# Kernel tuning notes

Measured on AMD Instinct MI355X. Metric: run time of the kernel, lower is better.

The kernel has to match this reference:

```python
import jax, jax.numpy as jnp
import numpy as np

B, S, D_MODEL, H = 2, 2048, 1024, 16
HD = D_MODEL // H  # 64
EPS = 1e-6


def setup_inputs() -> dict:
    key = jax.random.key(0)
    ks = jax.random.split(key, 8)
    x = jax.random.normal(ks[0], (B, S, D_MODEL), dtype=jnp.float32)
    # Proper RoPE rotation angles: theta_i = pos / 10000^(2i/head_dim)
    inv_freq = 1.0 / (10000.0 ** (np.arange(0, HD, 2, dtype=np.float32) / HD))  # (HD/2,)
    angles = np.arange(S, dtype=np.float32)[:, None] * inv_freq[None, :]        # (S, HD/2)
    rope_cos = jnp.asarray(np.cos(angles))
    rope_sin = jnp.asarray(np.sin(angles))
    w_std = 1.0 / np.sqrt(D_MODEL)
    wq = jax.random.normal(ks[1], (D_MODEL, D_MODEL), dtype=jnp.float32) * w_std
    wk = jax.random.normal(ks[2], (D_MODEL, D_MODEL), dtype=jnp.float32) * w_std
    wv = jax.random.normal(ks[3], (D_MODEL, D_MODEL), dtype=jnp.float32) * w_std
    wo = jax.random.normal(ks[4], (D_MODEL, D_MODEL), dtype=jnp.float32) * w_std
    q_scale = 1.0 + 0.02 * jax.random.normal(ks[5], (HD,), dtype=jnp.float32)
    k_scale = 1.0 + 0.02 * jax.random.normal(ks[6], (HD,), dtype=jnp.float32)
    return {"x": x, "wq": wq, "wk": wk, "wv": wv, "wo": wo,
            "q_scale": q_scale, "k_scale": k_scale,
            "rope_cos": rope_cos, "rope_sin": rope_sin}


def _rmsnorm(t, scale):
    # RMSNorm over head_dim
    var = jnp.mean(jnp.square(t), axis=-1, keepdims=True)
    return t * jax.lax.rsqrt(var + EPS) * scale


def _apply_rope(t, cos, sin):
    # t: (B,S,H,HD); interpret consecutive pairs as complex (real, imag)
    b, s, h, d = t.shape
    tp = t.reshape(b, s, h, d // 2, 2)
    tr, ti = tp[..., 0], tp[..., 1]
    c = cos[None, :, None, :]  # (1,S,1,HD/2)
    sn = sin[None, :, None, :]
    or_ = tr * c - ti * sn
    oi = tr * sn + ti * c
    return jnp.stack([or_, oi], axis=-1).reshape(b, s, h, d)


def reference(x, wq, wk, wv, wo, q_scale, k_scale, rope_cos, rope_sin):
    b, s, _ = x.shape
    # Torch-style linear: y = x @ W^T, W is (out, in)
    q = jnp.einsum('bsd,od->bso', x, wq).reshape(b, s, H, HD)
    k = jnp.einsum('bsd,od->bso', x, wk).reshape(b, s, H, HD)
    v = jnp.einsum('bsd,od->bso', x, wv).reshape(b, s, H, HD)
    q = _apply_rope(_rmsnorm(q, q_scale), rope_cos, rope_sin)
    k = _apply_rope(_rmsnorm(k, k_scale), rope_cos, rope_sin)
    # scaled dot-product attention (no mask), fp32 softmax
    scale = 1.0 / np.sqrt(HD)
    scores = jnp.einsum('bqhd,bkhd->bhqk', q, k) * scale
    probs = jax.nn.softmax(scores.astype(jnp.float32), axis=-1)
    attn = jnp.einsum('bhqk,bkhd->bqhd', probs, v).reshape(b, s, D_MODEL)
    return jnp.einsum('bso,do->bsd', attn, wo.T).astype(x.dtype) if False else jnp.einsum('bsd,od->bso', attn, wo)
```

## Files before the change

kernel.cpp:

```cpp
#include <hip/hip_runtime.h>
#include <hip/hip_bf16.h>


#define B_ 2
#define S_ 2048
#define D_ 1024
#define H_ 16
#define HD_ 64
#define M_ (B_*S_)
#define SPLIT_ 2
#define KSPAN_ (S_/SPLIT_)

typedef __attribute__((ext_vector_type(8))) short short8;
typedef __attribute__((ext_vector_type(4))) short short4v;
typedef __attribute__((ext_vector_type(4))) float f32x4;
typedef __attribute__((ext_vector_type(4))) _Float16 half4;
typedef __attribute__((ext_vector_type(8))) _Float16 half8;

static __device__ __forceinline__ short f2bf(float f) {
    __hip_bfloat16 h = __float2bfloat16(f);
    return *reinterpret_cast<short*>(&h);
}
static __device__ __forceinline__ short f2h(float f) {
    _Float16 h = (_Float16)f;
    return *reinterpret_cast<short*>(&h);
}

typedef __attribute__((address_space(1))) const unsigned int gu32_t;
typedef __attribute__((address_space(3))) unsigned int lu32_t;
static __device__ __forceinline__ void gld16(const short* g, short* l) {
    __builtin_amdgcn_global_load_lds((gu32_t*)g, (lu32_t*)l, 16, 0, 0);
}

__global__ __launch_bounds__(256)
void convert_bf16(const float* __restrict__ x,
                  const float* __restrict__ wq, const float* __restrict__ wk,
                  const float* __restrict__ wv, const float* __restrict__ wo,
                  short* __restrict__ xb, short* __restrict__ wqkvb, short* __restrict__ wob)
{
    const size_t t4 = ((size_t)blockIdx.x * 256 + threadIdx.x) * 4;
    const float* src; short* dst; size_t off, doff;
    if (t4 < 4194304)      { src = x;  dst = xb;    off = t4;           doff = t4; }
    else if (t4 < 5242880) { src = wq; dst = wqkvb; off = t4 - 4194304; doff = t4 - 4194304; }
    else if (t4 < 6291456) { src = wk; dst = wqkvb; off = t4 - 5242880; doff = t4 - 4194304; }
    else if (t4 < 7340032) { src = wv; dst = wqkvb; off = t4 - 6291456; doff = t4 - 4194304; }
    else                   { src = wo; dst = wob;   off = t4 - 7340032; doff = t4 - 7340032; }
    float4 v = *(const float4*)(src + off);
    short4v s = { f2bf(v.x), f2bf(v.y), f2bf(v.z), f2bf(v.w) };
    *(short4v*)(dst + doff) = s;
}

__global__ __launch_bounds__(256)
void gemm_qkv(const short* __restrict__ A, const short* __restrict__ Bw,
              short* __restrict__ Qb, short* __restrict__ Kb, short* __restrict__ Vt,
              const float* __restrict__ q_scale, const float* __restrict__ k_scale,
              const float* __restrict__ rope_cos, const float* __restrict__ rope_sin)
{
    __shared__ __align__(16) short As[2][128*64];
    __shared__ __align__(16) short Bs[2][128*64];
    const int tid = threadIdx.x;
    const int w = tid >> 6, lane = tid & 63, quad = lane >> 4, l16 = lane & 15;
    const int wr = w >> 1, wc = w & 1;
    const int bm0 = blockIdx.x * 128, bn0 = blockIdx.y * 128;

    const int row_ = tid >> 3;
    const int kslot = tid & 7;
    const short* gA[4]; const short* gB[4];
    #pragma unroll
    for (int j = 0; j < 4; ++j) {
        const int row = j*32 + row_;
        const int kch = kslot ^ (row & 7);
        gA[j] = A  + (size_t)(bm0 + row) * 1024 + kch*8;
        gB[j] = Bw + (size_t)(bn0 + row) * 1024 + kch*8;
    }

    f32x4 acc[4][4];
    #pragma unroll
    for (int i = 0; i < 4; ++i)
        #pragma unroll
        for (int j = 0; j < 4; ++j) acc[i][j] = (f32x4){0.f,0.f,0.f,0.f};

    #pragma unroll
    for (int j = 0; j < 4; ++j) {
        gld16(gA[j], &As[0][j*2048 + w*512]);
        gld16(gB[j], &Bs[0][j*2048 + w*512]);
    }
    asm volatile("s_waitcnt vmcnt(0)" ::: "memory");
    __builtin_amdgcn_s_barrier();
    __builtin_amdgcn_sched_barrier(0);

    int cur = 0;
    for (int t = 0; t < 16; ++t) {
        if (t < 15) {
            const int k0 = (t + 1) * 64;
            #pragma unroll
            for (int j = 0; j < 4; ++j) {
                gld16(gA[j] + k0, &As[cur ^ 1][j*2048 + w*512]);
                gld16(gB[j] + k0, &Bs[cur ^ 1][j*2048 + w*512]);
            }
        }
        __builtin_amdgcn_sched_barrier(0);

        short8 af[2][4], bfr[2][4];
        #pragma unroll
        for (int ph = 0; ph < 2; ++ph)
            #pragma unroll
            for (int i = 0; i < 4; ++i) {
                const int ra = wr*64 + i*16 + l16;
                af[ph][i]  = *(const short8*)(&As[cur][ra*64 + (((ph*4 + quad) ^ (ra & 7)) << 3)]);
                const int rb = wc*64 + i*16 + l16;
                bfr[ph][i] = *(const short8*)(&Bs[cur][rb*64 + (((ph*4 + quad) ^ (rb & 7)) << 3)]);
            }
        #pragma unroll
        for (int ph = 0; ph < 2; ++ph)
            #pragma unroll
            for (int i = 0; i < 4; ++i)
                #pragma unroll
                for (int j = 0; j < 4; ++j)
                    acc[i][j] = __builtin_amdgcn_mfma_f32_16x16x32_bf16(af[ph][i], bfr[ph][j], acc[i][j], 0, 0, 0);

        asm volatile("s_waitcnt vmcnt(0)" ::: "memory");
        __builtin_amdgcn_s_barrier();
        __builtin_amdgcn_sched_barrier(0);
        cur ^= 1;
    }

    const int nbase = bn0 + wc*64;
    const int which = nbase >> 10;
    const int h     = (nbase & 1023) >> 6;

    if (which < 2) {
        const float* sc = which ? k_scale : q_scale;
        short* dst      = which ? Kb : Qb;
        const float fold = which ? 1.0f : 0.18033688011112042f;
        float scv[4];
        #pragma unroll
        for (int j = 0; j < 4; ++j) scv[j] = sc[j*16 + l16];
        #pragma unroll
        for (int i = 0; i < 4; ++i) {
            #pragma unroll
            for (int r = 0; r < 4; ++r) {
                const int m = bm0 + wr*64 + i*16 + quad*4 + r;
                const int b = m >> 11, s = m & (S_-1);
                float ss = 0.f;
                #pragma unroll
                for (int j = 0; j < 4; ++j) ss += acc[i][j][r] * acc[i][j][r];
                #pragma unroll
                for (int msk = 1; msk <= 8; msk <<= 1) ss += __shfl_xor(ss, msk, 64);
                const float rn = rsqrtf(ss * (1.0f/64.0f) + 1e-6f);
                #pragma unroll
                for (int j = 0; j < 4; ++j) {
                    const int hd = j*16 + l16;
                    const float nv = acc[i][j][r] * rn * scv[j];
                    const float c  = rope_cos[s*32 + (hd >> 1)];
                    const float sn = rope_sin[s*32 + (hd >> 1)];
                    const float partner = __shfl_xor(nv, 1, 64);
                    const float o = (hd & 1) ? (partner * sn + nv * c) : (nv * c - partner * sn);
                    dst[(((size_t)b*H_ + h)*S_ + s)*HD_ + hd] = f2bf(o * fold);
                }
            }
        }
    } else {
        #pragma unroll
        for (int i = 0; i < 4; ++i)
            #pragma unroll
            for (int r = 0; r < 4; ++r) {
                const int m = bm0 + wr*64 + i*16 + quad*4 + r;
                const int b = m >> 11, s = m & (S_-1);
                #pragma unroll
                for (int j = 0; j < 4; ++j) {
                    const int hd = j*16 + l16;
                    Vt[(((size_t)b*H_ + h)*HD_ + hd)*S_ + s] = f2h(acc[i][j][r]);
                }
            }
    }
}

__global__ __launch_bounds__(256)
void gemm_out(const short* __restrict__ po, const float* __restrict__ pl,
              const short* __restrict__ Bw, float* __restrict__ C)
{
    __shared__ __align__(16) short As[2][64*64];
    __shared__ __align__(16) short Bs[2][128*64];
    const int tid = threadIdx.x;
    const int w = tid >> 6, lane = tid & 63, quad = lane >> 4, l16 = lane & 15;
    const int bm0 = blockIdx.x * 64, bn0 = blockIdx.y * 128;

    const int row_ = tid >> 3;
    const int kslot = tid & 7;
    const short* gB[4];
    #pragma unroll
    for (int j = 0; j < 4; ++j) {
        const int row = j*32 + row_;
        const int kch = kslot ^ (row & 7);
        gB[j] = Bw + (size_t)(bn0 + row) * 1024 + kch*8;
    }

    const int srow = tid >> 2;
    const int ch0  = (tid & 3) * 2;
    const int m = bm0 + srow;
    const int b = m >> 11, s = m & (S_-1);
    const short* p0 = po +            (size_t)m * 1024;
    const short* p1 = po + 4194304 + (size_t)m * 1024;

    float inv[16];
    #pragma unroll
    for (int h = 0; h < 16; ++h)
        inv[h] = 1.0f / (pl[((size_t)(b*16 + h))*S_ + s] + pl[65536 + ((size_t)(b*16 + h))*S_ + s]);

    f32x4 acc[4][2];
    #pragma unroll
    for (int i = 0; i < 4; ++i) {
        acc[i][0] = (f32x4){0.f,0.f,0.f,0.f};
        acc[i][1] = (f32x4){0.f,0.f,0.f,0.f};
    }

    {
        half8 d00 = *(const half8*)(p0 + ch0*8);
        half8 d01 = *(const half8*)(p1 + ch0*8);
        half8 d10 = *(const half8*)(p0 + ch0*8 + 8);
        half8 d11 = *(const half8*)(p1 + ch0*8 + 8);
        #pragma unroll
        for (int j = 0; j < 4; ++j)
            gld16(gB[j], &Bs[0][j*2048 + w*512]);
        const float invh = inv[0];
        short8 a0, a1;
        #pragma unroll
        for (int j = 0; j < 8; ++j) {
            a0[j] = f2bf(((float)d00[j] + (float)d01[j]) * invh);
            a1[j] = f2bf(((float)d10[j] + (float)d11[j]) * invh);
        }
        *(short8*)(&As[0][srow*64 + (((ch0    ) ^ (srow & 7)) << 3)]) = a0;
        *(short8*)(&As[0][srow*64 + (((ch0 + 1) ^ (srow & 7)) << 3)]) = a1;
        asm volatile("s_waitcnt vmcnt(0) lgkmcnt(0)" ::: "memory");
        __builtin_amdgcn_s_barrier();
        __builtin_amdgcn_sched_barrier(0);
    }

    int cur = 0;
    #pragma unroll
    for (int t = 0; t < 16; ++t) {
        half8 d00, d01, d10, d11;
        if (t < 15) {
            const int k0 = (t + 1) * 64;
            d00 = *(const half8*)(p0 + k0 + ch0*8);
            d01 = *(const half8*)(p1 + k0 + ch0*8);
            d10 = *(const half8*)(p0 + k0 + ch0*8 + 8);
            d11 = *(const half8*)(p1 + k0 + ch0*8 + 8);
            #pragma unroll
            for (int j = 0; j < 4; ++j)
                gld16(gB[j] + k0, &Bs[cur ^ 1][j*2048 + w*512]);
        }
        __builtin_amdgcn_sched_barrier(0);

        #pragma unroll
        for (int ph = 0; ph < 2; ++ph) {
            short8 af[4], bfr[2];
            #pragma unroll
            for (int i = 0; i < 4; ++i) {
                const int ra = i*16 + l16;
                af[i] = *(const short8*)(&As[cur][ra*64 + (((ph*4 + quad) ^ (ra & 7)) << 3)]);
            }
            #pragma unroll
            for (int j = 0; j < 2; ++j) {
                const int rb = w*32 + j*16 + l16;
                bfr[j] = *(const short8*)(&Bs[cur][rb*64 + (((ph*4 + quad) ^ (rb & 7)) << 3)]);
            }
            #pragma unroll
            for (int i = 0; i < 4; ++i)
                #pragma unroll
                for (int j = 0; j < 2; ++j)
                    acc[i][j] = __builtin_amdgcn_mfma_f32_16x16x32_bf16(af[i], bfr[j], acc[i][j], 0, 0, 0);
        }

        if (t < 15) {
            asm volatile("s_waitcnt vmcnt(0)" ::: "memory");
            const float invh = inv[t + 1];
            short8 a0, a1;
            #pragma unroll
            for (int j = 0; j < 8; ++j) {
                a0[j] = f2bf(((float)d00[j] + (float)d01[j]) * invh);
                a1[j] = f2bf(((float)d10[j] + (float)d11[j]) * invh);
            }
            *(short8*)(&As[cur ^ 1][srow*64 + (((ch0    ) ^ (srow & 7)) << 3)]) = a0;
            *(short8*)(&As[cur ^ 1][srow*64 + (((ch0 + 1) ^ (srow & 7)) << 3)]) = a1;
            asm volatile("s_waitcnt lgkmcnt(0)" ::: "memory");
            __builtin_amdgcn_s_barrier();
            __builtin_amdgcn_sched_barrier(0);
            cur ^= 1;
        }
    }

    #pragma unroll
    for (int i = 0; i < 4; ++i)
        #pragma unroll
        for (int r = 0; r < 4; ++r) {
            const int mm = bm0 + i*16 + quad*4 + r;
            #pragma unroll
            for (int j = 0; j < 2; ++j) {
                const int n = bn0 + w*32 + j*16 + l16;
                C[(size_t)mm*1024 + n] = acc[i][j][r];
            }
        }
}

__global__ __launch_bounds__(256)
void flash_mfma(const short* __restrict__ qb, const short* __restrict__ kb,
                const short* __restrict__ vt, short* __restrict__ po, float* __restrict__ pl)
{
    __shared__ __align__(16) short Ks[64*64];
    __shared__ __align__(16) short Vs[64*64];

    const int id   = blockIdx.x;
    const int xcd  = id & 7;
    const int rest = id >> 3;
    const int qblk = rest & 7;
    const int g    = (rest >> 3) * 8 + xcd;
    const int bh   = g >> 1;
    const int sp   = g & 1;

    const int tid  = threadIdx.x;
    const int wv   = tid >> 6;
    const int lane = tid & 63;
    const int quad = lane >> 4;
    const int l16  = lane & 15;
    const int b    = bh >> 4, h = bh & (H_-1);
    const int q0   = qblk * 256 + wv * 64;
    const int kt0  = sp * KSPAN_;
    const size_t hbase = (size_t)bh * S_ * HD_;
    const size_t vbase = (size_t)bh * HD_ * S_;
    short* po_sp = po + (size_t)sp * 4194304;
    float* pl_sp = pl + (size_t)sp * 65536;

    const int c0r = tid >> 3,       c0c = tid & 7;
    const int c1r = (tid+256) >> 3, c1c = (tid+256) & 7;

    short8 qfrag[4][2];
    #pragma unroll
    for (int qf = 0; qf < 4; ++qf)
        #pragma unroll
        for (int c = 0; c < 2; ++c)
            qfrag[qf][c] = *(const short8*)(qb + hbase + (size_t)(q0 + qf*16 + l16)*HD_ + c*32 + quad*8);

    f32x4 Oacc[4][4];
    #pragma unroll
    for (int qf = 0; qf < 4; ++qf)
        #pragma unroll
        for (int dt = 0; dt < 4; ++dt) Oacc[qf][dt] = (f32x4){0.f,0.f,0.f,0.f};
    float l_lane[4] = {0.f, 0.f, 0.f, 0.f};

    short8 rk0 = *(const short8*)(kb + hbase + (size_t)(kt0 + c0r)*HD_ + c0c*8);
    short8 rk1 = *(const short8*)(kb + hbase + (size_t)(kt0 + c1r)*HD_ + c1c*8);
    short8 rv0 = *(const short8*)(vt + vbase + (size_t)c0r*S_ + kt0 + c0c*8);
    short8 rv1 = *(const short8*)(vt + vbase + (size_t)c1r*S_ + kt0 + c1c*8);

    #pragma unroll 1
    for (int t = 0; t < KSPAN_/64; ++t) {
        __syncthreads();
        *(short8*)(Ks + c0r*64 + ((c0c ^ (c0r & 7)) << 3)) = rk0;
        *(short8*)(Ks + c1r*64 + ((c1c ^ (c1r & 7)) << 3)) = rk1;
        *(short8*)(Vs + c0r*64 + ((c0c ^ (c0r & 7)) << 3)) = rv0;
        *(short8*)(Vs + c1r*64 + ((c1c ^ (c1r & 7)) << 3)) = rv1;
        __syncthreads();
        if (t < KSPAN_/64 - 1) {
            const int ktn = kt0 + (t+1)*64;
            rk0 = *(const short8*)(kb + hbase + (size_t)(ktn + c0r)*HD_ + c0c*8);
            rk1 = *(const short8*)(kb + hbase + (size_t)(ktn + c1r)*HD_ + c1c*8);
            rv0 = *(const short8*)(vt + vbase + (size_t)c0r*S_ + ktn + c0c*8);
            rv1 = *(const short8*)(vt + vbase + (size_t)c1r*S_ + ktn + c1c*8);
        }

        #pragma unroll
        for (int st = 0; st < 4; ++st) {
            short8 kf0 = *(const short8*)(Ks + (st*16 + l16)*64 + (((quad    ) ^ (l16 & 7)) << 3));
            short8 kf1 = *(const short8*)(Ks + (st*16 + l16)*64 + (((4 + quad) ^ (l16 & 7)) << 3));
            const int ch16 = st*2 + (quad >> 1);
            const int sw   = ((ch16 ^ (l16 & 7)) << 3) + (quad & 1)*4;
            half4 va[4];
            #pragma unroll
            for (int dt = 0; dt < 4; ++dt)
                va[dt] = *(const half4*)(Vs + (dt*16 + l16)*64 + sw);
            #pragma unroll
            for (int qf = 0; qf < 4; ++qf) {
                f32x4 acc = (f32x4){0.f,0.f,0.f,0.f};
                acc = __builtin_amdgcn_mfma_f32_16x16x32_bf16(kf0, qfrag[qf][0], acc, 0, 0, 0);
                acc = __builtin_amdgcn_mfma_f32_16x16x32_bf16(kf1, qfrag[qf][1], acc, 0, 0, 0);
                half4 pb;
                #pragma unroll
                for (int r = 0; r < 4; ++r) {
                    float p = __builtin_amdgcn_exp2f(acc[r] - 12.0f);
                    l_lane[qf] += p;
                    pb[r] = (_Float16)p;
                }
                #pragma unroll
                for (int dt = 0; dt < 4; ++dt)
                    Oacc[qf][dt] = __builtin_amdgcn_mfma_f32_16x16x16f16(va[dt], pb, Oacc[qf][dt], 0, 0, 0);
            }
        }
    }

    #pragma unroll
    for (int qf = 0; qf < 4; ++qf) {
        l_lane[qf] += __shfl_xor(l_lane[qf], 16, 64);
        l_lane[qf] += __shfl_xor(l_lane[qf], 32, 64);
        if (quad == 0) pl_sp[(size_t)bh*S_ + q0 + qf*16 + l16] = l_lane[qf];
    }
    #pragma unroll
    for (int qf = 0; qf < 4; ++qf) {
        const int s = q0 + qf*16 + l16;
        #pragma unroll
        for (int dt = 0; dt < 4; ++dt) {
            short4v o;
            #pragma unroll
            for (int r = 0; r < 4; ++r) o[r] = f2h(Oacc[qf][dt][r]);
            *(short4v*)(po_sp + (((size_t)b*S_ + s)*H_ + h)*HD_ + dt*16 + quad*4) = o;
        }
    }
}

extern "C" void kernel_launch(void* const* d_in, const int* in_sizes, int n_in,
                              void* d_out, int out_size, void* d_ws, size_t ws_size,
                              hipStream_t stream)
{
    (void)in_sizes; (void)n_in; (void)out_size; (void)ws_size;
    const float* x        = (const float*)d_in[0];
    const float* wq       = (const float*)d_in[1];
    const float* wk       = (const float*)d_in[2];
    const float* wv       = (const float*)d_in[3];
    const float* wo       = (const float*)d_in[4];
    const float* q_scale  = (const float*)d_in[5];
    const float* k_scale  = (const float*)d_in[6];
    const float* rope_cos = (const float*)d_in[7];
    const float* rope_sin = (const float*)d_in[8];
    float* out = (float*)d_out;
    short* ws  = (short*)d_ws;

    short* qbh   = ws;
    short* kbh   = ws + 4194304;
    short* vt    = ws + 8388608;
    short* xb    = ws + 16777216;
    short* wqkvb = ws + 20971520;
    short* wob   = ws + 24117248;
    short* po    = ws + 25165824;
    float* pl    = (float*)(ws + 33554432);

    convert_bf16<<<dim3(8192), 256, 0, stream>>>(x, wq, wk, wv, wo, xb, wqkvb, wob);
    gemm_qkv<<<dim3(M_/128, 24), 256, 0, stream>>>(xb, wqkvb, qbh, kbh, vt,
                                                   q_scale, k_scale, rope_cos, rope_sin);
    flash_mfma<<<dim3((S_/256)*B_*H_*SPLIT_), 256, 0, stream>>>(qbh, kbh, vt, po, pl);
    gemm_out<<<dim3(M_/64, D_/128), 256, 0, stream>>>(po, pl, wob, out);
}
```

Measured before the change: 202.1 us.

## Increase flash-attention KV split to four and relocate partial buffers in workspace

Doubles the number of key/value splits in the flash-attention kernel, so twice as many blocks run, each over a shorter key span. The aim is higher occupancy and better load balance across the compute units. The four fp16 partial outputs and their row sums now live in workspace regions that are free after the QKV GEMM (the gap after Vt, the xb region and the wqkvb region), located through a constant offset table. In exchange, the output GEMM must read and sum four partials instead of two, which doubles its partial-output memory traffic, and each split block pays the Q-load and setup overhead over less work.

```diff
diff --git a/kernel.cpp b/kernel.cpp
--- a/kernel.cpp
+++ b/kernel.cpp
@@ -8,7 +8,7 @@
 #define H_ 16
 #define HD_ 64
 #define M_ (B_*S_)
-#define SPLIT_ 2
+#define SPLIT_ 4
 #define KSPAN_ (S_/SPLIT_)
 
 typedef __attribute__((ext_vector_type(8))) short short8;
@@ -31,6 +31,9 @@
 static __device__ __forceinline__ void gld16(const short* g, short* l) {
     __builtin_amdgcn_global_load_lds((gu32_t*)g, (lu32_t*)l, 16, 0, 0);
 }
+
+__device__ __constant__ int PO_OFF[4] = {25165824, 29360128, 12582912, 16777216};
+#define PL_OFF_ 20971520
 
 __global__ __launch_bounds__(256)
 void convert_bf16(const float* __restrict__ x,
@@ -177,8 +180,7 @@
 }
 
 __global__ __launch_bounds__(256)
-void gemm_out(const short* __restrict__ po, const float* __restrict__ pl,
-              const short* __restrict__ Bw, float* __restrict__ C)
+void gemm_out(const short* __restrict__ wsall, const short* __restrict__ Bw, float* __restrict__ C)
 {
     __shared__ __align__(16) short As[2][64*64];
     __shared__ __align__(16) short Bs[2][128*64];
@@ -200,13 +202,21 @@
     const int ch0  = (tid & 3) * 2;
     const int m = bm0 + srow;
     const int b = m >> 11, s = m & (S_-1);
-    const short* p0 = po +            (size_t)m * 1024;
-    const short* p1 = po + 4194304 + (size_t)m * 1024;
+    const short* p[4];
+    #pragma unroll
+    for (int sp = 0; sp < 4; ++sp)
+        p[sp] = wsall + PO_OFF[sp] + (size_t)m * 1024;
+    const float* pl = (const float*)(wsall + PL_OFF_);
 
     float inv[16];
     #pragma unroll
-    for (int h = 0; h < 16; ++h)
-        inv[h] = 1.0f / (pl[((size_t)(b*16 + h))*S_ + s] + pl[65536 + ((size_t)(b*16 + h))*S_ + s]);
+    for (int h = 0; h < 16; ++h) {
+        float d = 0.f;
+        #pragma unroll
+        for (int sp = 0; sp < 4; ++sp)
+            d += pl[sp*65536 + ((size_t)(b*16 + h))*S_ + s];
+        inv[h] = 1.0f / d;
+    }
 
     f32x4 acc[4][2];
     #pragma unroll
@@ -216,10 +226,12 @@
     }
 
     {
-        half8 d00 = *(const half8*)(p0 + ch0*8);
-        half8 d01 = *(const half8*)(p1 + ch0*8);
-        half8 d10 = *(const half8*)(p0 + ch0*8 + 8);
-        half8 d11 = *(const half8*)(p1 + ch0*8 + 8);
+        half8 d0[4], d1[4];
+        #pragma unroll
+        for (int sp = 0; sp < 4; ++sp) {
+            d0[sp] = *(const half8*)(p[sp] + ch0*8);
+            d1[sp] = *(const half8*)(p[sp] + ch0*8 + 8);
+        }
         #pragma unroll
         for (int j = 0; j < 4; ++j)
             gld16(gB[j], &Bs[0][j*2048 + w*512]);
@@ -227,8 +239,8 @@
         short8 a0, a1;
         #pragma unroll
         for (int j = 0; j < 8; ++j) {
-            a0[j] = f2bf(((float)d00[j] + (float)d01[j]) * invh);
-            a1[j] = f2bf(((float)d10[j] + (float)d11[j]) * invh);
+            a0[j] = f2bf(((float)d0[0][j] + (float)d0[1][j] + (float)d0[2][j] + (float)d0[3][j]) * invh);
+            a1[j] = f2bf(((float)d1[0][j] + (float)d1[1][j] + (float)d1[2][j] + (float)d1[3][j]) * invh);
         }
         *(short8*)(&As[0][srow*64 + (((ch0    ) ^ (srow & 7)) << 3)]) = a0;
         *(short8*)(&As[0][srow*64 + (((ch0 + 1) ^ (srow & 7)) << 3)]) = a1;
@@ -240,13 +252,14 @@
     int cur = 0;
     #pragma unroll
     for (int t = 0; t < 16; ++t) {
-        half8 d00, d01, d10, d11;
+        half8 d0[4], d1[4];
         if (t < 15) {
             const int k0 = (t + 1) * 64;
-            d00 = *(const half8*)(p0 + k0 + ch0*8);
-            d01 = *(const half8*)(p1 + k0 + ch0*8);
-            d10 = *(const half8*)(p0 + k0 + ch0*8 + 8);
-            d11 = *(const half8*)(p1 + k0 + ch0*8 + 8);
+            #pragma unroll
+            for (int sp = 0; sp < 4; ++sp) {
+                d0[sp] = *(const half8*)(p[sp] + k0 + ch0*8);
+                d1[sp] = *(const half8*)(p[sp] + k0 + ch0*8 + 8);
+            }
             #pragma unroll
             for (int j = 0; j < 4; ++j)
                 gld16(gB[j] + k0, &Bs[cur ^ 1][j*2048 + w*512]);
@@ -279,8 +292,8 @@
             short8 a0, a1;
             #pragma unroll
             for (int j = 0; j < 8; ++j) {
-                a0[j] = f2bf(((float)d00[j] + (float)d01[j]) * invh);
-                a1[j] = f2bf(((float)d10[j] + (float)d11[j]) * invh);
+                a0[j] = f2bf(((float)d0[0][j] + (float)d0[1][j] + (float)d0[2][j] + (float)d0[3][j]) * invh);
+                a1[j] = f2bf(((float)d1[0][j] + (float)d1[1][j] + (float)d1[2][j] + (float)d1[3][j]) * invh);
             }
             *(short8*)(&As[cur ^ 1][srow*64 + (((ch0    ) ^ (srow & 7)) << 3)]) = a0;
             *(short8*)(&As[cur ^ 1][srow*64 + (((ch0 + 1) ^ (srow & 7)) << 3)]) = a1;
@@ -306,7 +319,7 @@
 
 __global__ __launch_bounds__(256)
 void flash_mfma(const short* __restrict__ qb, const short* __restrict__ kb,
-                const short* __restrict__ vt, short* __restrict__ po, float* __restrict__ pl)
+                const short* __restrict__ vt, short* __restrict__ wsall)
 {
     __shared__ __align__(16) short Ks[64*64];
     __shared__ __align__(16) short Vs[64*64];
@@ -316,8 +329,8 @@
     const int rest = id >> 3;
     const int qblk = rest & 7;
     const int g    = (rest >> 3) * 8 + xcd;
-    const int bh   = g >> 1;
-    const int sp   = g & 1;
+    const int bh   = g >> 2;
+    const int sp   = g & 3;
 
     const int tid  = threadIdx.x;
     const int wv   = tid >> 6;
@@ -329,8 +342,8 @@
     const int kt0  = sp * KSPAN_;
     const size_t hbase = (size_t)bh * S_ * HD_;
     const size_t vbase = (size_t)bh * HD_ * S_;
-    short* po_sp = po + (size_t)sp * 4194304;
-    float* pl_sp = pl + (size_t)sp * 65536;
+    short* po_sp = wsall + PO_OFF[sp];
+    float* pl_sp = (float*)(wsall + PL_OFF_) + (size_t)sp * 65536;
 
     const int c0r = tid >> 3,       c0c = tid & 7;
     const int c1r = (tid+256) >> 3, c1c = (tid+256) & 7;
@@ -441,12 +454,10 @@
     short* xb    = ws + 16777216;
     short* wqkvb = ws + 20971520;
     short* wob   = ws + 24117248;
-    short* po    = ws + 25165824;
-    float* pl    = (float*)(ws + 33554432);
 
     convert_bf16<<<dim3(8192), 256, 0, stream>>>(x, wq, wk, wv, wo, xb, wqkvb, wob);
     gemm_qkv<<<dim3(M_/128, 24), 256, 0, stream>>>(xb, wqkvb, qbh, kbh, vt,
                                                    q_scale, k_scale, rope_cos, rope_sin);
-    flash_mfma<<<dim3((S_/256)*B_*H_*SPLIT_), 256, 0, stream>>>(qbh, kbh, vt, po, pl);
-    gemm_out<<<dim3(M_/64, D_/128), 256, 0, stream>>>(po, pl, wob, out);
-}
+    flash_mfma<<<dim3((S_/256)*B_*H_*SPLIT_), 256, 0, stream>>>(qbh, kbh, vt, ws);
+    gemm_out<<<dim3(M_/64, D_/128), 256, 0, stream>>>(ws, wob, out);
+}
```

After: 212.0 us. 4.9% more time.
